# Kernel tuning notes

Hardware: AMD Instinct MI355X
Metric: run time of the kernel (lower is better)

Reference implementation:

```python
import jax, jax.numpy as jnp
import numpy as np

D_MODEL = 1024
D_STATE = 16
D_CONV = 4
EXPAND = 2
D_INNER = EXPAND * D_MODEL  # 2048
BATCH = 2
SEQ = 2048


def setup_inputs() -> dict:
    key = jax.random.key(0)
    ks = jax.random.split(key, 7)
    s = 0.02
    x = jax.random.normal(ks[0], (BATCH, SEQ, D_MODEL), jnp.float32)
    in_proj_w = jax.random.normal(ks[1], (2 * D_INNER, D_MODEL), jnp.float32) * s
    conv_w = jax.random.normal(ks[2], (D_INNER, 1, D_CONV), jnp.float32) * s  # depthwise: groups=d_inner
    conv_b = jnp.zeros((D_INNER,), jnp.float32)
    x_proj_w = jax.random.normal(ks[3], (2 * D_STATE, D_INNER), jnp.float32) * s
    dt_proj_w = jax.random.normal(ks[4], (D_INNER, D_INNER), jnp.float32) * s
    dt_proj_b = jnp.zeros((D_INNER,), jnp.float32)
    # A = arange(1..d_state) repeated for each inner channel; A_log = log(A)
    A_log = jnp.log(jnp.tile(jnp.arange(1, D_STATE + 1, dtype=jnp.float32), (D_INNER, 1)))
    D_param = jnp.ones((D_INNER,), jnp.float32)
    out_proj_w = jax.random.normal(ks[5], (D_MODEL, D_INNER), jnp.float32) * s
    return {"x": x, "in_proj_w": in_proj_w, "conv_w": conv_w, "conv_b": conv_b,
            "x_proj_w": x_proj_w, "dt_proj_w": dt_proj_w, "dt_proj_b": dt_proj_b,
            "A_log": A_log, "D_param": D_param, "out_proj_w": out_proj_w}


def reference(x, in_proj_w, conv_w, conv_b, x_proj_w, dt_proj_w, dt_proj_b, A_log, D_param, out_proj_w):
    B, L, _ = x.shape
    # input projection -> [B, L, 2*d_inner], split into ssm path and gate
    xz = x @ in_proj_w.T
    x_ssm, z = jnp.split(xz, 2, axis=-1)

    # causal depthwise conv1d (torch pads both sides by d_conv-1 then slices [:L])
    xc = jnp.transpose(x_ssm, (0, 2, 1))  # [B, d_inner, L]
    xc = jnp.pad(xc, ((0, 0), (0, 0), (D_CONV - 1, 0)))
    xc = jax.lax.conv_general_dilated(
        xc, conv_w, window_strides=(1,), padding='VALID',
        dimension_numbers=('NCH', 'OIH', 'NCH'), feature_group_count=D_INNER)
    xc = xc + conv_b[None, :, None]
    x_act = jax.nn.silu(jnp.transpose(xc, (0, 2, 1)))  # [B, L, d_inner]

    delta = jax.nn.softplus(x_act @ dt_proj_w.T + dt_proj_b)  # [B, L, d_inner]
    bc = x_act @ x_proj_w.T                                   # [B, L, 2*d_state]
    B_p, C_p = jnp.split(bc, 2, axis=-1)

    A = -jnp.exp(A_log)  # [d_inner, d_state]

    def step(h, inp):
        u_i, d_i, B_i, C_i = inp  # [B,d], [B,d], [B,n], [B,n]
        dA = jnp.exp(d_i[..., None] * A)                       # [B, d, n]
        h = dA * h + (d_i * u_i)[..., None] * B_i[:, None, :]  # [B, d, n]
        y = jnp.einsum('bdn,bn->bd', h, C_i)
        return h, y

    h0 = jnp.zeros((B, D_INNER, D_STATE), x.dtype)
    seq = (jnp.swapaxes(x_act, 0, 1), jnp.swapaxes(delta, 0, 1),
           jnp.swapaxes(B_p, 0, 1), jnp.swapaxes(C_p, 0, 1))
    _, ys = jax.lax.scan(step, h0, seq)  # ys: [L, B, d_inner]
    y_ssm = jnp.swapaxes(ys, 0, 1) + x_act * D_param

    y = y_ssm * jax.nn.silu(z)
    return y @ out_proj_w.T
```

## Files before the change

kernel.cpp:

```cpp
#include <hip/hip_runtime.h>
#include <hip/hip_bf16.h>
#include <math.h>

#define DM 1024
#define DS 16
#define DI 2048
#define NB 2
#define LL 2048
#define BL (NB*LL)
#define LC 32
#define NC (LL/LC)

typedef __attribute__((ext_vector_type(8))) short short8;
typedef __attribute__((ext_vector_type(8))) unsigned short ushort8;
typedef __attribute__((ext_vector_type(4))) float f32x4;

__device__ __forceinline__ float silu_f(float x){ return x / (1.f + __expf(-x)); }
__device__ __forceinline__ float softplus_f(float x){ return (x > 15.f) ? x : log1pf(__expf(x)); }
__device__ __forceinline__ unsigned short f2bf(float f){
  unsigned u = __float_as_uint(f);
  u += 0x7fff + ((u >> 16) & 1);
  return (unsigned short)(u >> 16);
}
__device__ __forceinline__ float bf2f(unsigned short v){
  return __uint_as_float(((unsigned)v) << 16);
}

__global__ __launch_bounds__(256) void f2b_k(const float* __restrict__ src,
                                             unsigned short* __restrict__ dst, int n)
{
  int i = (blockIdx.x * 256 + threadIdx.x) * 8;
  if (i >= n) return;
  float4 v0 = *(const float4*)&src[i];
  float4 v1 = *(const float4*)&src[i + 4];
  ushort8 o;
  o[0]=f2bf(v0.x); o[1]=f2bf(v0.y); o[2]=f2bf(v0.z); o[3]=f2bf(v0.w);
  o[4]=f2bf(v1.x); o[5]=f2bf(v1.y); o[6]=f2bf(v1.z); o[7]=f2bf(v1.w);
  *(ushort8*)&dst[i] = o;
}

template<int EPI>
__global__ __launch_bounds__(256) void gemm_bt_mfma(
    const unsigned short* __restrict__ A, const unsigned short* __restrict__ Bw,
    const float* __restrict__ bias, float* __restrict__ C,
    int M, int N, int K)
{
  __shared__ unsigned short As[128 * 32];
  __shared__ unsigned short Bs[128 * 32];
  const int t = threadIdx.x;
  const int wid = t >> 6, lane = t & 63;
  const int bm = blockIdx.y * 128, bn = blockIdx.x * 128;
  const int wm = (wid >> 1) * 64, wn = (wid & 1) * 64;
  f32x4 acc[4][4] = {};

  const int srow = (lane >> 2);
  const int scol = (lane & 3) * 8;

  for (int k0 = 0; k0 < K; k0 += 32) {
    __syncthreads();
    #pragma unroll
    for (int q = 0; q < 2; q++) {
      int seg = wid * 2 + q;
      int row = seg * 16 + srow;
      __builtin_amdgcn_global_load_lds(
          (const __attribute__((address_space(1))) void*)(A + (size_t)(bm + row) * K + k0 + scol),
          (__attribute__((address_space(3))) void*)(As + seg * 512), 16, 0, 0);
      __builtin_amdgcn_global_load_lds(
          (const __attribute__((address_space(1))) void*)(Bw + (size_t)(bn + row) * K + k0 + scol),
          (__attribute__((address_space(3))) void*)(Bs + seg * 512), 16, 0, 0);
    }
    __syncthreads();
    short8 af[4], bfr[4];
    #pragma unroll
    for (int i = 0; i < 4; i++) {
      af[i]  = *(const short8*)&As[(wm + i * 16 + (lane & 15)) * 32 + (lane >> 4) * 8];
      bfr[i] = *(const short8*)&Bs[(wn + i * 16 + (lane & 15)) * 32 + (lane >> 4) * 8];
    }
    #pragma unroll
    for (int i = 0; i < 4; i++)
      #pragma unroll
      for (int j = 0; j < 4; j++)
        acc[i][j] = __builtin_amdgcn_mfma_f32_16x16x32_bf16(af[i], bfr[j], acc[i][j], 0, 0, 0);
  }
  #pragma unroll
  for (int i = 0; i < 4; i++) {
    #pragma unroll
    for (int j = 0; j < 4; j++) {
      int col = bn + wn + j * 16 + (lane & 15);
      #pragma unroll
      for (int r = 0; r < 4; r++) {
        int row = bm + wm + i * 16 + (lane >> 4) * 4 + r;
        float v = acc[i][j][r];
        if (EPI == 1) v = softplus_f(v + bias[col]);
        C[(size_t)row * N + col] = v;
      }
    }
  }
}

__global__ __launch_bounds__(256) void conv_silu_k(
    const float* __restrict__ xz, const float* __restrict__ cw,
    const float* __restrict__ cb, unsigned short* __restrict__ xa)
{
  int idx = blockIdx.x * 256 + threadIdx.x;
  int d  = idx & (DI - 1);
  int bl = idx >> 11;
  int l  = bl & (LL - 1);
  float acc = cb[d];
  #pragma unroll
  for (int k = 0; k < 4; k++) {
    int ls = l - 3 + k;
    if (ls >= 0)
      acc += xz[((size_t)(bl - l + ls)) * (2 * DI) + d] * cw[d * 4 + k];
  }
  xa[idx] = f2bf(silu_f(acc));
}

__global__ __launch_bounds__(256) void bc_k(
    const unsigned short* __restrict__ xa, const unsigned short* __restrict__ w,
    float* __restrict__ bc)
{
  __shared__ unsigned short sx[8 * DI];
  const int t = threadIdx.x;
  const size_t base = (size_t)blockIdx.x * 8 * DI;
  #pragma unroll
  for (int it = 0; it < 8; it++) {
    int v = t + it * 256;
    *(ushort8*)&sx[v * 8] = *(const ushort8*)&xa[base + (size_t)v * 8];
  }
  __syncthreads();
  const int m = t >> 5, n = t & 31;
  const unsigned short* wr = w + (size_t)n * DI;
  const unsigned short* xr = sx + m * DI;
  float acc = 0.f;
  #pragma unroll 4
  for (int k = 0; k < DI; k += 8) {
    ushort8 xv = *(const ushort8*)&xr[k];
    ushort8 wv = *(const ushort8*)&wr[k];
    #pragma unroll
    for (int j = 0; j < 8; j++) acc += bf2f(xv[j]) * bf2f(wv[j]);
  }
  bc[(size_t)(blockIdx.x * 8 + m) * 32 + n] = acc;
}

__global__ __launch_bounds__(256) void scan_part1(
    const float* __restrict__ dlt, const unsigned short* __restrict__ xa,
    const float* __restrict__ bc, const float* __restrict__ A_log,
    float* __restrict__ S_arr, float* __restrict__ sumdlt)
{
  const int bid = blockIdx.x;
  const int b = bid >> 9;
  const int c = (bid >> 3) & (NC - 1);
  const int dg = bid & 7;
  const int t = threadIdx.x;
  const int d = dg * 256 + t;
  float Ac[16];
  #pragma unroll
  for (int n = 0; n < 16; n++) Ac[n] = -__expf(A_log[d * 16 + n]);
  __shared__ float sB[LC][16];
  for (int e = t; e < LC * 16; e += 256) {
    int l = e >> 4, n = e & 15;
    sB[l][n] = bc[(size_t)(b * LL + c * LC + l) * 32 + n];
  }
  __syncthreads();
  float h[16] = {};
  float sd = 0.f;
  size_t rowbase = (size_t)(b * LL + c * LC) * DI + d;
  for (int l = 0; l < LC; l++) {
    float dl = dlt[rowbase + (size_t)l * DI];
    float u  = bf2f(xa[rowbase + (size_t)l * DI]);
    float w = dl * u;
    sd += dl;
    #pragma unroll
    for (int n = 0; n < 16; n++) {
      float dA = __expf(dl * Ac[n]);
      h[n] = dA * h[n] + w * sB[l][n];
    }
  }
  float* Sp = S_arr + ((size_t)(b * NC + c) * DI + d) * 16;
  #pragma unroll
  for (int n = 0; n < 16; n++) Sp[n] = h[n];
  sumdlt[(size_t)(b * NC + c) * DI + d] = sd;
}

__global__ __launch_bounds__(256) void scan_combine(
    const float* __restrict__ A_log, const float* __restrict__ sumdlt,
    float* __restrict__ S_arr)
{
  int tid = blockIdx.x * 256 + threadIdx.x;
  int n = tid & 15;
  int d = (tid >> 4) & (DI - 1);
  int b = tid >> 15;
  float Ac = -__expf(A_log[d * 16 + n]);
  float h = 0.f;
  for (int c = 0; c < NC; c++) {
    size_t idx = ((size_t)(b * NC + c) * DI + d) * 16 + n;
    float S = S_arr[idx];
    float P = __expf(sumdlt[(size_t)(b * NC + c) * DI + d] * Ac);
    S_arr[idx] = h;
    h = P * h + S;
  }
}

__global__ __launch_bounds__(256) void scan_part2(
    const float* __restrict__ dlt, const unsigned short* __restrict__ xa,
    const float* __restrict__ bc, const float* __restrict__ A_log,
    const float* __restrict__ Dp, const float* __restrict__ xz,
    const float* __restrict__ Hin, unsigned short* __restrict__ y)
{
  const int bid = blockIdx.x;
  const int b = bid >> 9;
  const int c = (bid >> 3) & (NC - 1);
  const int dg = bid & 7;
  const int t = threadIdx.x;
  const int d = dg * 256 + t;
  float Ac[16];
  #pragma unroll
  for (int n = 0; n < 16; n++) Ac[n] = -__expf(A_log[d * 16 + n]);
  __shared__ float sB[LC][16];
  __shared__ float sC[LC][16];
  for (int e = t; e < LC * 16; e += 256) {
    int l = e >> 4, n = e & 15;
    size_t row = (size_t)(b * LL + c * LC + l) * 32;
    sB[l][n] = bc[row + n];
    sC[l][n] = bc[row + 16 + n];
  }
  __syncthreads();
  float h[16];
  const float* Hp = Hin + ((size_t)(b * NC + c) * DI + d) * 16;
  #pragma unroll
  for (int n = 0; n < 16; n++) h[n] = Hp[n];
  const float Dv = Dp[d];
  size_t rowbase = (size_t)(b * LL + c * LC) * DI + d;
  for (int l = 0; l < LC; l++) {
    float dl = dlt[rowbase + (size_t)l * DI];
    float u  = bf2f(xa[rowbase + (size_t)l * DI]);
    float w = dl * u;
    float ya = 0.f;
    #pragma unroll
    for (int n = 0; n < 16; n++) {
      float dA = __expf(dl * Ac[n]);
      h[n] = dA * h[n] + w * sB[l][n];
      ya += h[n] * sC[l][n];
    }
    float zz = xz[(size_t)(b * LL + c * LC + l) * (2 * DI) + DI + d];
    y[rowbase + (size_t)l * DI] = f2bf((ya + u * Dv) * silu_f(zz));
  }
}

extern "C" void kernel_launch(void* const* d_in, const int* in_sizes, int n_in,
                              void* d_out, int out_size, void* d_ws, size_t ws_size,
                              hipStream_t stream)
{
  const float* x    = (const float*)d_in[0];
  const float* Win  = (const float*)d_in[1];
  const float* cw   = (const float*)d_in[2];
  const float* cb   = (const float*)d_in[3];
  const float* Wxp  = (const float*)d_in[4];
  const float* Wdt  = (const float*)d_in[5];
  const float* bdt  = (const float*)d_in[6];
  const float* Alog = (const float*)d_in[7];
  const float* Dp   = (const float*)d_in[8];
  const float* Wout = (const float*)d_in[9];
  float* out = (float*)d_out;

  float* ws = (float*)d_ws;
  float* xz     = ws;
  float* dlt    = xz + 16777216;
  float* bcb    = dlt + 8388608;
  float* S_arr  = bcb + 131072;
  float* sumdlt = S_arr + 4194304;
  unsigned short* xa_bf = (unsigned short*)(sumdlt + 262144);
  unsigned short* y_bf  = xa_bf + 8388608;
  unsigned short* x_bf  = y_bf;
  unsigned short* wbuf  = y_bf + 8388608;
  unsigned short* wxp_bf= wbuf + 4194304;

  dim3 blk(256);
  f2b_k<<<dim3(BL*DM/2048), blk, 0, stream>>>(x, x_bf, BL*DM);
  f2b_k<<<dim3(2*DI*DM/2048), blk, 0, stream>>>(Win, wbuf, 2*DI*DM);
  gemm_bt_mfma<0><<<dim3((2*DI)/128, BL/128), blk, 0, stream>>>(x_bf, wbuf, nullptr, xz, BL, 2*DI, DM);
  conv_silu_k<<<dim3((BL*DI)/256), blk, 0, stream>>>(xz, cw, cb, xa_bf);
  f2b_k<<<dim3(DI*DI/2048), blk, 0, stream>>>(Wdt, wbuf, DI*DI);
  gemm_bt_mfma<1><<<dim3(DI/128, BL/128), blk, 0, stream>>>(xa_bf, wbuf, bdt, dlt, BL, DI, DI);
  f2b_k<<<dim3(2*DS*DI/2048), blk, 0, stream>>>(Wxp, wxp_bf, 2*DS*DI);
  bc_k<<<dim3(BL/8), blk, 0, stream>>>(xa_bf, wxp_bf, bcb);
  scan_part1<<<dim3(NB*NC*8), blk, 0, stream>>>(dlt, xa_bf, bcb, Alog, S_arr, sumdlt);
  scan_combine<<<dim3(NB*DI*DS/256), blk, 0, stream>>>(Alog, sumdlt, S_arr);
  scan_part2<<<dim3(NB*NC*8), blk, 0, stream>>>(dlt, xa_bf, bcb, Alog, Dp, xz, S_arr, y_bf);
  f2b_k<<<dim3(DM*DI/2048), blk, 0, stream>>>(Wout, wbuf, DM*DI);
  gemm_bt_mfma<0><<<dim3(DM/128, BL/128), blk, 0, stream>>>(y_bf, wbuf, nullptr, out, BL, DM, DI);
}
```

Before: 378.2 us.

## Rewrite GEMMs with 256-row tiles, double-buffered LDS, swizzle, bf16 xz output

```diff
diff --git a/kernel.cpp b/kernel.cpp
--- a/kernel.cpp
+++ b/kernel.cpp
@@ -39,67 +39,99 @@
   *(ushort8*)&dst[i] = o;
 }
 
-template<int EPI>
-__global__ __launch_bounds__(256) void gemm_bt_mfma(
+template<int BN, int EPI, int OUTBF>
+__global__ __launch_bounds__(512, 2) void gemm2(
     const unsigned short* __restrict__ A, const unsigned short* __restrict__ Bw,
-    const float* __restrict__ bias, float* __restrict__ C,
+    const float* __restrict__ bias, void* __restrict__ Cp,
     int M, int N, int K)
 {
-  __shared__ unsigned short As[128 * 32];
-  __shared__ unsigned short Bs[128 * 32];
+  constexpr int BM = 256;
+  constexpr int NR = BN / 64;
+  __shared__ unsigned short lds[2][(BM + BN) * 64];
   const int t = threadIdx.x;
   const int wid = t >> 6, lane = t & 63;
-  const int bm = blockIdx.y * 128, bn = blockIdx.x * 128;
-  const int wm = (wid >> 1) * 64, wn = (wid & 1) * 64;
-  f32x4 acc[4][4] = {};
-
-  const int srow = (lane >> 2);
-  const int scol = (lane & 3) * 8;
-
-  for (int k0 = 0; k0 < K; k0 += 32) {
+  const int nbx = N / BN;
+  const int cpx = (nbx * (M / BM)) >> 3;
+  const int bid = (int)blockIdx.x;
+  const int swz = (bid & 7) * cpx + (bid >> 3);
+  const int bm = (swz / nbx) * BM, bn = (swz % nbx) * BN;
+  const int wm = (wid >> 2) * 128, wn = (wid & 3) * (BN / 4);
+  const int srow8 = lane >> 3;
+  const int sch   = lane & 7;
+
+  f32x4 acc[8][NR] = {};
+
+  auto stage = [&](int buf, int k0) {
+    #pragma unroll
+    for (int p = 0; p < BM / 64; p++) {
+      int row = p * 64 + wid * 8 + srow8;
+      int ch = sch ^ (row & 7);
+      __builtin_amdgcn_global_load_lds(
+        (const __attribute__((address_space(1))) void*)(A + (size_t)(bm + row) * K + k0 + ch * 8),
+        (__attribute__((address_space(3))) void*)(&lds[buf][(p * 64 + wid * 8) * 64]), 16, 0, 0);
+    }
+    #pragma unroll
+    for (int p = 0; p < BN / 64; p++) {
+      int row = p * 64 + wid * 8 + srow8;
+      int ch = sch ^ (row & 7);
+      __builtin_amdgcn_global_load_lds(
+        (const __attribute__((address_space(1))) void*)(Bw + (size_t)(bn + row) * K + k0 + ch * 8),
+        (__attribute__((address_space(3))) void*)(&lds[buf][(BM + p * 64 + wid * 8) * 64]), 16, 0, 0);
+    }
+  };
+
+  stage(0, 0);
+  __syncthreads();
+  const int nk = K / 64;
+  int cur = 0;
+  for (int kt = 0; kt < nk; kt++) {
+    if (kt + 1 < nk) stage(cur ^ 1, (kt + 1) * 64);
+    const unsigned short* bufA = &lds[cur][0];
+    const unsigned short* bufB = &lds[cur][BM * 64];
+    #pragma unroll
+    for (int ks = 0; ks < 2; ks++) {
+      short8 af[8], bfr[NR];
+      #pragma unroll
+      for (int i = 0; i < 8; i++) {
+        int r = wm + i * 16 + (lane & 15);
+        int c = ((ks << 2) + (lane >> 4)) ^ (r & 7);
+        af[i] = *(const short8*)&bufA[r * 64 + c * 8];
+      }
+      #pragma unroll
+      for (int j = 0; j < NR; j++) {
+        int r = wn + j * 16 + (lane & 15);
+        int c = ((ks << 2) + (lane >> 4)) ^ (r & 7);
+        bfr[j] = *(const short8*)&bufB[r * 64 + c * 8];
+      }
+      #pragma unroll
+      for (int i = 0; i < 8; i++)
+        #pragma unroll
+        for (int j = 0; j < NR; j++)
+          acc[i][j] = __builtin_amdgcn_mfma_f32_16x16x32_bf16(af[i], bfr[j], acc[i][j], 0, 0, 0);
+    }
     __syncthreads();
-    #pragma unroll
-    for (int q = 0; q < 2; q++) {
-      int seg = wid * 2 + q;
-      int row = seg * 16 + srow;
-      __builtin_amdgcn_global_load_lds(
-          (const __attribute__((address_space(1))) void*)(A + (size_t)(bm + row) * K + k0 + scol),
-          (__attribute__((address_space(3))) void*)(As + seg * 512), 16, 0, 0);
-      __builtin_amdgcn_global_load_lds(
-          (const __attribute__((address_space(1))) void*)(Bw + (size_t)(bn + row) * K + k0 + scol),
-          (__attribute__((address_space(3))) void*)(Bs + seg * 512), 16, 0, 0);
-    }
-    __syncthreads();
-    short8 af[4], bfr[4];
-    #pragma unroll
-    for (int i = 0; i < 4; i++) {
-      af[i]  = *(const short8*)&As[(wm + i * 16 + (lane & 15)) * 32 + (lane >> 4) * 8];
-      bfr[i] = *(const short8*)&Bs[(wn + i * 16 + (lane & 15)) * 32 + (lane >> 4) * 8];
-    }
-    #pragma unroll
-    for (int i = 0; i < 4; i++)
-      #pragma unroll
-      for (int j = 0; j < 4; j++)
-        acc[i][j] = __builtin_amdgcn_mfma_f32_16x16x32_bf16(af[i], bfr[j], acc[i][j], 0, 0, 0);
-  }
-  #pragma unroll
-  for (int i = 0; i < 4; i++) {
-    #pragma unroll
-    for (int j = 0; j < 4; j++) {
+    cur ^= 1;
+  }
+  #pragma unroll
+  for (int i = 0; i < 8; i++) {
+    #pragma unroll
+    for (int j = 0; j < NR; j++) {
       int col = bn + wn + j * 16 + (lane & 15);
+      float bv = (EPI == 1) ? bias[col] : 0.f;
       #pragma unroll
       for (int r = 0; r < 4; r++) {
         int row = bm + wm + i * 16 + (lane >> 4) * 4 + r;
         float v = acc[i][j][r];
-        if (EPI == 1) v = softplus_f(v + bias[col]);
-        C[(size_t)row * N + col] = v;
+        if (EPI == 1) v = softplus_f(v + bv);
+        if (OUTBF) ((unsigned short*)Cp)[(size_t)row * N + col] = f2bf(v);
+        else       ((float*)Cp)[(size_t)row * N + col] = v;
       }
     }
   }
 }
 
 __global__ __launch_bounds__(256) void conv_silu_k(
-    const float* __restrict__ xz, const float* __restrict__ cw,
+    const unsigned short* __restrict__ xz, const float* __restrict__ cw,
     const float* __restrict__ cb, unsigned short* __restrict__ xa)
 {
   int idx = blockIdx.x * 256 + threadIdx.x;
@@ -111,7 +143,7 @@
   for (int k = 0; k < 4; k++) {
     int ls = l - 3 + k;
     if (ls >= 0)
-      acc += xz[((size_t)(bl - l + ls)) * (2 * DI) + d] * cw[d * 4 + k];
+      acc += bf2f(xz[((size_t)(bl - l + ls)) * (2 * DI) + d]) * cw[d * 4 + k];
   }
   xa[idx] = f2bf(silu_f(acc));
 }
@@ -205,7 +237,7 @@
 __global__ __launch_bounds__(256) void scan_part2(
     const float* __restrict__ dlt, const unsigned short* __restrict__ xa,
     const float* __restrict__ bc, const float* __restrict__ A_log,
-    const float* __restrict__ Dp, const float* __restrict__ xz,
+    const float* __restrict__ Dp, const unsigned short* __restrict__ xz,
     const float* __restrict__ Hin, unsigned short* __restrict__ y)
 {
   const int bid = blockIdx.x;
@@ -243,7 +275,7 @@
       h[n] = dA * h[n] + w * sB[l][n];
       ya += h[n] * sC[l][n];
     }
-    float zz = xz[(size_t)(b * LL + c * LC + l) * (2 * DI) + DI + d];
+    float zz = bf2f(xz[(size_t)(b * LL + c * LC + l) * (2 * DI) + DI + d]);
     y[rowbase + (size_t)l * DI] = f2bf((ya + u * Dv) * silu_f(zz));
   }
 }
@@ -265,12 +297,12 @@
   float* out = (float*)d_out;
 
   float* ws = (float*)d_ws;
-  float* xz     = ws;
-  float* dlt    = xz + 16777216;
+  float* dlt    = ws;
   float* bcb    = dlt + 8388608;
   float* S_arr  = bcb + 131072;
   float* sumdlt = S_arr + 4194304;
-  unsigned short* xa_bf = (unsigned short*)(sumdlt + 262144);
+  unsigned short* xz_bf = (unsigned short*)(sumdlt + 262144);
+  unsigned short* xa_bf = xz_bf + 16777216;
   unsigned short* y_bf  = xa_bf + 8388608;
   unsigned short* x_bf  = y_bf;
   unsigned short* wbuf  = y_bf + 8388608;
@@ -279,15 +311,15 @@
   dim3 blk(256);
   f2b_k<<<dim3(BL*DM/2048), blk, 0, stream>>>(x, x_bf, BL*DM);
   f2b_k<<<dim3(2*DI*DM/2048), blk, 0, stream>>>(Win, wbuf, 2*DI*DM);
-  gemm_bt_mfma<0><<<dim3((2*DI)/128, BL/128), blk, 0, stream>>>(x_bf, wbuf, nullptr, xz, BL, 2*DI, DM);
-  conv_silu_k<<<dim3((BL*DI)/256), blk, 0, stream>>>(xz, cw, cb, xa_bf);
+  gemm2<256,0,1><<<dim3(256), dim3(512), 0, stream>>>(x_bf, wbuf, nullptr, xz_bf, BL, 2*DI, DM);
+  conv_silu_k<<<dim3((BL*DI)/256), blk, 0, stream>>>(xz_bf, cw, cb, xa_bf);
   f2b_k<<<dim3(DI*DI/2048), blk, 0, stream>>>(Wdt, wbuf, DI*DI);
-  gemm_bt_mfma<1><<<dim3(DI/128, BL/128), blk, 0, stream>>>(xa_bf, wbuf, bdt, dlt, BL, DI, DI);
+  gemm2<128,1,0><<<dim3(256), dim3(512), 0, stream>>>(xa_bf, wbuf, bdt, dlt, BL, DI, DI);
   f2b_k<<<dim3(2*DS*DI/2048), blk, 0, stream>>>(Wxp, wxp_bf, 2*DS*DI);
   bc_k<<<dim3(BL/8), blk, 0, stream>>>(xa_bf, wxp_bf, bcb);
   scan_part1<<<dim3(NB*NC*8), blk, 0, stream>>>(dlt, xa_bf, bcb, Alog, S_arr, sumdlt);
   scan_combine<<<dim3(NB*DI*DS/256), blk, 0, stream>>>(Alog, sumdlt, S_arr);
-  scan_part2<<<dim3(NB*NC*8), blk, 0, stream>>>(dlt, xa_bf, bcb, Alog, Dp, xz, S_arr, y_bf);
+  scan_part2<<<dim3(NB*NC*8), blk, 0, stream>>>(dlt, xa_bf, bcb, Alog, Dp, xz_bf, S_arr, y_bf);
   f2b_k<<<dim3(DM*DI/2048), blk, 0, stream>>>(Wout, wbuf, DM*DI);
-  gemm_bt_mfma<0><<<dim3(DM/128, BL/128), blk, 0, stream>>>(y_bf, wbuf, nullptr, out, BL, DM, DI);
-}
+  gemm2<64,0,0><<<dim3(256), dim3(512), 0, stream>>>(y_bf, wbuf, nullptr, out, BL, DM, DI);
+}
```

Result: faster. 325.0 us (-14.1%).
